# Kernel tuning notes

Measured on AMD Instinct MI355X. Metric: run time of the kernel, lower is better.

The kernel has to match this reference:

```python
import jax, jax.numpy as jnp
import numpy as np

# --- architecture constants (match init_kwargs) ---
SLEN = 104
PTILE = 8
STEP = 2
N_BANDS = 2
MAX_DET = 2
N_SRC_PARAMS = 2
ENC_C = 20
ENC_HIDDEN = 256
# dim_out_all = 0.5*D*(D+1)*(4+2*n_source_params) + 1 + D  (probs over n_sources + per-count loc/flux mean+logvar)
DIM_OUT = int(0.5 * MAX_DET * (MAX_DET + 1) * (4 + 2 * N_SRC_PARAMS)) + 1 + MAX_DET  # 27


def _p(key, shape, scale=0.02):
    return scale * jax.random.normal(key, shape, dtype=jnp.float32)


def setup_inputs() -> dict:
    key = jax.random.key(0)
    ks = jax.random.split(key, 14)
    flat_in = ENC_C * PTILE * PTILE  # 20*8*8 = 1280
    return {
        "images": jax.random.normal(ks[0], (32, N_BANDS, SLEN, SLEN), dtype=jnp.float32),
        "conv1_w": _p(ks[1], (ENC_C, N_BANDS, 3, 3)),
        "conv1_b": _p(ks[2], (ENC_C,)),
        "conv2_w": _p(ks[3], (ENC_C, ENC_C, 3, 3)),
        "conv2_b": _p(ks[4], (ENC_C,)),
        "fc1_w": _p(ks[5], (ENC_HIDDEN, flat_in)),
        "fc1_b": _p(ks[6], (ENC_HIDDEN,)),
        "fc2_w": _p(ks[7], (ENC_HIDDEN, ENC_HIDDEN)),
        "fc2_b": _p(ks[8], (ENC_HIDDEN,)),
        "fc3_w": _p(ks[9], (ENC_HIDDEN, ENC_HIDDEN)),
        "fc3_b": _p(ks[10], (ENC_HIDDEN,)),
        "fcf_w": _p(ks[11], (DIM_OUT, ENC_HIDDEN)),
        "fcf_b": _p(ks[12], (DIM_OUT,)),
    }


def _tile_images(images):
    # torch tile_images: (B, C, slen, slen) -> (B * n_ptiles, C, P, P), tiles row-major over (x, y)
    B, C = images.shape[0], images.shape[1]
    patches = jax.lax.conv_general_dilated_patches(
        images, filter_shape=(PTILE, PTILE), window_strides=(STEP, STEP), padding="VALID"
    )  # (B, C*P*P, Hn, Wn) with feature dim ordered (C, P, P)
    Hn, Wn = patches.shape[2], patches.shape[3]
    p = patches.reshape(B, C, PTILE, PTILE, Hn, Wn)
    p = p.transpose(0, 4, 5, 1, 2, 3)  # (B, Hn, Wn, C, P, P)
    return p.reshape(B * Hn * Wn, C, PTILE, PTILE)


def _conv(x, w, b):
    y = jax.lax.conv_general_dilated(
        x, w, window_strides=(1, 1), padding="SAME",
        dimension_numbers=("NCHW", "OIHW", "NCHW"),
    )
    return y + b[None, :, None, None]


def reference(images, conv1_w, conv1_b, conv2_w, conv2_b,
              fc1_w, fc1_b, fc2_w, fc2_b, fc3_w, fc3_b, fcf_w, fcf_b):
    ptiles = _tile_images(images)                       # (B*nT, C, P, P)
    h = jax.nn.relu(_conv(ptiles, conv1_w, conv1_b))    # (B*nT, 20, P, P)
    h = jax.nn.relu(_conv(h, conv2_w, conv2_b))
    h = h.reshape(h.shape[0], -1)                       # Flatten -> (B*nT, 1280)
    h = jax.nn.relu(h @ fc1_w.T + fc1_b)
    h = jax.nn.relu(h @ fc2_w.T + fc2_b)
    h = jax.nn.relu(h @ fc3_w.T + fc3_b)
    return h @ fcf_w.T + fcf_b                          # (B*nT, dim_out_all)
```

## Files before the change

kernel.cpp:

```cpp
#include <hip/hip_runtime.h>
#include <hip/hip_bf16.h>

#define NPATCH 76832
#define NBLK   601
#define K1     1280

typedef __attribute__((ext_vector_type(8))) short  short8;
typedef __attribute__((ext_vector_type(4))) float  floatx4;

__device__ __forceinline__ unsigned short f2b(float f) {
    unsigned int u = __builtin_bit_cast(unsigned int, f);
    u += 0x7FFFu + ((u >> 16) & 1u);
    return (unsigned short)(u >> 16);
}
__device__ __forceinline__ unsigned int pk2(float a, float b) {
    __hip_bfloat162 h = __float22bfloat162_rn(make_float2(a, b));
    unsigned int u;
    __builtin_memcpy(&u, &h, 4);
    return u;
}

__device__ __forceinline__ void gload_lds16(const unsigned short* g, unsigned short* l) {
    __builtin_amdgcn_global_load_lds(
        (__attribute__((address_space(1))) void*)g,
        (__attribute__((address_space(3))) void*)l,
        16, 0, 0);
}

__device__ __host__ __forceinline__ int swz8(int row, int i) {
    return (((row & 1) * 4 + i) ^ ((row >> 1) & 7));
}

__global__ void prep(const float* __restrict__ f1w, const float* __restrict__ f2w,
                     const float* __restrict__ f3w, const float* __restrict__ c1w,
                     const float* __restrict__ c2w, const float* __restrict__ ffw,
                     unsigned short* __restrict__ W1F, unsigned short* __restrict__ W2F,
                     unsigned short* __restrict__ W3F, unsigned short* __restrict__ W1T,
                     unsigned short* __restrict__ W2T, unsigned short* __restrict__ WfF) {
    int i = blockIdx.x * 256 + threadIdx.x;
    if (i < 327680) {
        int o = i / 1280, k = i - o * 1280;
        int dst = ((k >> 5) * 16 + (o >> 6) * 4 + ((o >> 4) & 3)) * 512
                + (((k >> 3) & 3) * 16 + (o & 15)) * 8 + (k & 7);
        W1F[dst] = f2b(f1w[i]);
        return;
    }
    i -= 327680;
    if (i < 65536) {
        int o = i >> 8, k = i & 255;
        int dst = ((k >> 5) * 16 + (o >> 6) * 4 + ((o >> 4) & 3)) * 512
                + (((k >> 3) & 3) * 16 + (o & 15)) * 8 + (k & 7);
        W2F[dst] = f2b(f2w[i]);
        return;
    }
    i -= 65536;
    if (i < 65536) {
        int o = i >> 8, k = i & 255;
        int dst = ((k >> 5) * 16 + (o >> 6) * 4 + ((o >> 4) & 3)) * 512
                + (((k >> 3) & 3) * 16 + (o & 15)) * 8 + (k & 7);
        W3F[dst] = f2b(f3w[i]);
        return;
    }
    i -= 65536;
    if (i < 1024) {
        int o = i >> 5, k = i & 31;
        unsigned short v = 0;
        if (o < 20 && k < 18) v = f2b(c1w[o * 18 + k]);
        W1T[(o >> 1) * 64 + swz8(o, k >> 3) * 8 + (k & 7)] = v;
        return;
    }
    i -= 1024;
    if (i < 9216) {
        int tap = i >> 10, rem = i & 1023, o = rem >> 5, c = rem & 31;
        unsigned short v = 0;
        if (o < 20 && c < 20) v = f2b(c2w[o * 180 + c * 9 + tap]);
        W2T[tap * 1024 + (o >> 1) * 64 + swz8(o, c >> 3) * 8 + (c & 7)] = v;
        return;
    }
    i -= 9216;
    if (i < 8192) {
        int o = i >> 8, k = i & 255;
        unsigned short v = (o < 27) ? f2b(ffw[o * 256 + k]) : (unsigned short)0;
        int dst = ((k >> 5) * 2 + (o >> 4)) * 512
                + (((k >> 3) & 3) * 16 + (o & 15)) * 8 + (k & 7);
        WfF[dst] = v;
    }
}

__global__ __launch_bounds__(256, 3) void conv_mfma(
    const float* __restrict__ img,
    const unsigned short* __restrict__ W1T, const float* __restrict__ b1,
    const unsigned short* __restrict__ W2T, const float* __restrict__ b2,
    unsigned short* __restrict__ X, int row0)
{
    __shared__ alignas(16) unsigned short s_buf[8 * 2048 + 64];
    __shared__ alignas(16) unsigned short s_w1t[1024];
    __shared__ alignas(16) unsigned short s_w2t[9216];
    __shared__ float s_b1[32], s_b2[32];
    constexpr int ZOFF = 8 * 2048;

    const int tid = threadIdx.x;
    for (int d = tid; d < 512; d += 256)  ((unsigned int*)s_w1t)[d] = ((const unsigned int*)W1T)[d];
    for (int d = tid; d < 4608; d += 256) ((unsigned int*)s_w2t)[d] = ((const unsigned int*)W2T)[d];
    if (tid < 32) {
        ((unsigned int*)&s_buf[ZOFF])[tid] = 0u;
        s_b1[tid] = (tid < 20) ? b1[tid] : 0.f;
        s_b2[tid] = (tid < 20) ? b2[tid] : 0.f;
    }

    const int q = tid >> 5, t = tid & 31;
    const int Pl = blockIdx.x * 8 + q;
    const int Pi = row0 + Pl;
    const bool valid = Pi < NPATCH;
    int b = 0, hi = 0, wi = 0;
    if (valid) { b = Pi / 2401; int rem = Pi - b * 2401; hi = rem / 49; wi = rem - hi * 49; }
    const int py = t >> 2, px0 = (t & 3) * 2;
    const float* ib = img + (long long)b * 21632 + (hi * 2) * 104 + (wi * 2);

    float win[2][3][4];
    #pragma unroll
    for (int c = 0; c < 2; ++c)
        #pragma unroll
        for (int dy = 0; dy < 3; ++dy) {
            int ny = py + dy - 1;
            int nyc = ny < 0 ? 0 : (ny > 7 ? 7 : ny);
            #pragma unroll
            for (int dxw = 0; dxw < 4; ++dxw) {
                int nx = px0 + dxw - 1;
                int nxc = nx < 0 ? 0 : (nx > 7 ? 7 : nx);
                win[c][dy][dxw] = ib[c * 10816 + nyc * 104 + nxc];
            }
        }

    #pragma unroll
    for (int j = 0; j < 2; ++j) {
        const int px = px0 + j, pl = py * 8 + px;
        float val[18];
        #pragma unroll
        for (int c = 0; c < 2; ++c)
            #pragma unroll
            for (int dy = 0; dy < 3; ++dy) {
                int ny = py + dy - 1;
                bool rok = valid && ((unsigned)ny < 8u);
                #pragma unroll
                for (int dx = 0; dx < 3; ++dx) {
                    int nx = px + dx - 1;
                    bool ok = rok && ((unsigned)nx < 8u);
                    val[c * 9 + dy * 3 + dx] = ok ? win[c][dy][dx + j] : 0.f;
                }
            }
        alignas(16) unsigned int au[16];
        #pragma unroll
        for (int i = 0; i < 9; ++i) au[i] = pk2(val[2 * i], val[2 * i + 1]);
        #pragma unroll
        for (int i = 9; i < 16; ++i) au[i] = 0u;
        unsigned short* base = &s_buf[q * 2048 + (pl >> 1) * 64];
        #pragma unroll
        for (int i = 0; i < 4; ++i)
            *(uint4*)&base[swz8(pl, i) * 8] = ((const uint4*)au)[i];
    }
    __syncthreads();

    const int wave = tid >> 6, lane = tid & 63;
    const int l15 = lane & 15, quad = lane >> 4;
    const int p0 = wave * 2;

    int boffB[2];
    #pragma unroll
    for (int i = 0; i < 2; ++i) {
        int oo = i * 16 + l15;
        boffB[i] = (oo >> 1) * 64 + swz8(oo, quad) * 8;
    }

    short8 a1f[2];
    #pragma unroll
    for (int mt = 0; mt < 2; ++mt) a1f[mt] = *(const short8*)&s_w1t[boffB[mt]];

    floatx4 acc1[2][2][4] = {};
    #pragma unroll
    for (int pp = 0; pp < 2; ++pp)
        #pragma unroll
        for (int nt = 0; nt < 4; ++nt) {
            int pix = nt * 16 + l15;
            short8 pf = *(const short8*)&s_buf[(p0 + pp) * 2048 + (pix >> 1) * 64 + swz8(pix, quad) * 8];
            #pragma unroll
            for (int mt = 0; mt < 2; ++mt)
                acc1[pp][mt][nt] = __builtin_amdgcn_mfma_f32_16x16x32_bf16(a1f[mt], pf, acc1[pp][mt][nt], 0, 0, 0);
        }

    float bv1[2][4];
    #pragma unroll
    for (int mt = 0; mt < 2; ++mt)
        #pragma unroll
        for (int r = 0; r < 4; ++r) bv1[mt][r] = s_b1[mt * 16 + quad * 4 + r];

    #pragma unroll
    for (int pp = 0; pp < 2; ++pp)
        #pragma unroll
        for (int mt = 0; mt < 2; ++mt)
            #pragma unroll
            for (int nt = 0; nt < 4; ++nt) {
                floatx4 v = acc1[pp][mt][nt];
                uint2 w;
                w.x = pk2(fmaxf(v[0] + bv1[mt][0], 0.f), fmaxf(v[1] + bv1[mt][1], 0.f));
                w.y = pk2(fmaxf(v[2] + bv1[mt][2], 0.f), fmaxf(v[3] + bv1[mt][3], 0.f));
                int pix = nt * 16 + l15;
                int off = (p0 + pp) * 2048 + (pix >> 1) * 64
                        + swz8(pix, mt * 2 + (quad >> 1)) * 8 + (quad & 1) * 4;
                *(uint2*)&s_buf[off] = w;
            }

    int syv[4], pxv[4];
    #pragma unroll
    for (int mt = 0; mt < 4; ++mt) { int p = mt * 16 + l15; syv[mt] = p >> 3; pxv[mt] = p & 7; }

    floatx4 acc2[2][4][2] = {};
    #pragma unroll 1
    for (int dy = 0; dy < 3; ++dy) {
        int sy[4]; bool okY[4];
        #pragma unroll
        for (int mt = 0; mt < 4; ++mt) {
            sy[mt] = syv[mt] + dy - 1;
            okY[mt] = (unsigned)sy[mt] < 8u;
        }
        #pragma unroll
        for (int dx = 0; dx < 3; ++dx) {
            const int tap = dy * 3 + dx;
            short8 bf0 = *(const short8*)&s_w2t[tap * 1024 + boffB[0]];
            short8 bf1 = *(const short8*)&s_w2t[tap * 1024 + boffB[1]];
            #pragma unroll
            for (int mt = 0; mt < 4; ++mt) {
                int sx = pxv[mt] + dx - 1;
                bool ok = okY[mt] & ((unsigned)sx < 8u);
                int ps = sy[mt] * 8 + sx;
                int offl = (ps >> 1) * 64 + swz8(ps, quad) * 8;
                #pragma unroll
                for (int pp = 0; pp < 2; ++pp) {
                    int off = ok ? ((p0 + pp) * 2048 + offl) : (ZOFF + quad * 8);
                    short8 af = *(const short8*)&s_buf[off];
                    acc2[pp][mt][0] = __builtin_amdgcn_mfma_f32_16x16x32_bf16(af, bf0, acc2[pp][mt][0], 0, 0, 0);
                    acc2[pp][mt][1] = __builtin_amdgcn_mfma_f32_16x16x32_bf16(af, bf1, acc2[pp][mt][1], 0, 0, 0);
                }
            }
        }
    }

    #pragma unroll
    for (int pp = 0; pp < 2; ++pp) {
        unsigned short* xrow = X + (long long)(blockIdx.x * 8 + p0 + pp) * K1;
        #pragma unroll
        for (int nt = 0; nt < 2; ++nt) {
            const int col = nt * 16 + l15;
            if (col < 20) {
                const float bv = s_b2[col];
                #pragma unroll
                for (int mt = 0; mt < 4; ++mt) {
                    floatx4 v = acc2[pp][mt][nt];
                    uint2 w;
                    w.x = pk2(fmaxf(v[0] + bv, 0.f), fmaxf(v[1] + bv, 0.f));
                    w.y = pk2(fmaxf(v[2] + bv, 0.f), fmaxf(v[3] + bv, 0.f));
                    *(uint2*)&xrow[col * 64 + mt * 16 + quad * 4] = w;
                }
            }
        }
    }
}

__global__ __launch_bounds__(256, 3) void fc_all(
    const unsigned short* __restrict__ X,
    const unsigned short* __restrict__ W1F, const unsigned short* __restrict__ W2F,
    const unsigned short* __restrict__ W3F, const unsigned short* __restrict__ WfF,
    const float* __restrict__ b1, const float* __restrict__ b2,
    const float* __restrict__ b3, const float* __restrict__ bf_,
    float* __restrict__ out, int row0)
{
    __shared__ alignas(16) unsigned short s_a[64 * 128];
    __shared__ alignas(16) unsigned short s_h[64 * 256];

    const int tid = threadIdx.x;
    const int m0 = blockIdx.x * 64;
    const int wave = tid >> 6, lane = tid & 63;
    const int l15 = lane & 15, quad = lane >> 4;

    floatx4 acc[4][4];
    #pragma unroll
    for (int mt = 0; mt < 4; ++mt)
        #pragma unroll
        for (int nt = 0; nt < 4; ++nt) acc[mt][nt] = floatx4{0.f, 0.f, 0.f, 0.f};

    #pragma unroll 1
    for (int kt = 0; kt < 1280; kt += 128) {
        #pragma unroll
        for (int i = 0; i < 4; ++i) {
            int g = i * 256 + tid;
            int row = g >> 4, pos = g & 15;
            int cc = (pos & 8) | ((pos & 7) ^ (row & 7));
            gload_lds16(X + (long long)(m0 + row) * 1280 + kt + cc * 8,
                        &s_a[i * 2048 + wave * 512]);
        }
        __syncthreads();
        #pragma unroll
        for (int kh = 0; kh < 4; ++kh) {
            const int khg = (kt >> 5) + kh;
            short8 af[4], bf[4];
            #pragma unroll
            for (int mt = 0; mt < 4; ++mt)
                af[mt] = *(const short8*)(W1F + (khg * 16 + wave * 4 + mt) * 512 + lane * 8);
            #pragma unroll
            for (int nt = 0; nt < 4; ++nt) {
                int row = nt * 16 + l15;
                int c = kh * 4 + quad;
                int pos = (c & 8) | ((c & 7) ^ (row & 7));
                bf[nt] = *(const short8*)&s_a[row * 128 + pos * 8];
            }
            #pragma unroll
            for (int mt = 0; mt < 4; ++mt)
                #pragma unroll
                for (int nt = 0; nt < 4; ++nt)
                    acc[mt][nt] = __builtin_amdgcn_mfma_f32_16x16x32_bf16(af[mt], bf[nt], acc[mt][nt], 0, 0, 0);
        }
        __syncthreads();
    }
    #pragma unroll
    for (int mt = 0; mt < 4; ++mt) {
        int obase = wave * 64 + mt * 16 + quad * 4;
        float v0 = b1[obase], v1 = b1[obase + 1], v2 = b1[obase + 2], v3 = b1[obase + 3];
        int clow = mt * 2 + (quad >> 1), sub = (quad & 1) * 4;
        #pragma unroll
        for (int nt = 0; nt < 4; ++nt) {
            int row = nt * 16 + l15;
            int pos = wave * 8 + (clow ^ (row & 7));
            floatx4 v = acc[mt][nt];
            uint2 w;
            w.x = pk2(fmaxf(v[0] + v0, 0.f), fmaxf(v[1] + v1, 0.f));
            w.y = pk2(fmaxf(v[2] + v2, 0.f), fmaxf(v[3] + v3, 0.f));
            *(uint2*)&s_h[row * 256 + pos * 8 + sub] = w;
        }
    }
    __syncthreads();

    #pragma unroll 1
    for (int layer = 0; layer < 2; ++layer) {
        const unsigned short* Wp = (layer == 0) ? W2F : W3F;
        const float* bp = (layer == 0) ? b2 : b3;

        #pragma unroll
        for (int mt = 0; mt < 4; ++mt)
            #pragma unroll
            for (int nt = 0; nt < 4; ++nt) acc[mt][nt] = floatx4{0.f, 0.f, 0.f, 0.f};

        #pragma unroll
        for (int it = 0; it < 8; ++it) {
            short8 af[4], bf[4];
            #pragma unroll
            for (int mt = 0; mt < 4; ++mt)
                af[mt] = *(const short8*)(Wp + (it * 16 + wave * 4 + mt) * 512 + lane * 8);
            int chi = it >> 1, clo4 = (it & 1) * 4 + quad;
            #pragma unroll
            for (int nt = 0; nt < 4; ++nt) {
                int row = nt * 16 + l15;
                bf[nt] = *(const short8*)&s_h[row * 256 + (chi * 8 + (clo4 ^ (row & 7))) * 8];
            }
            #pragma unroll
            for (int mt = 0; mt < 4; ++mt)
                #pragma unroll
                for (int nt = 0; nt < 4; ++nt)
                    acc[mt][nt] = __builtin_amdgcn_mfma_f32_16x16x32_bf16(af[mt], bf[nt], acc[mt][nt], 0, 0, 0);
        }
        __syncthreads();
        #pragma unroll
        for (int mt = 0; mt < 4; ++mt) {
            int obase = wave * 64 + mt * 16 + quad * 4;
            float v0 = bp[obase], v1 = bp[obase + 1], v2 = bp[obase + 2], v3 = bp[obase + 3];
            int clow = mt * 2 + (quad >> 1), sub = (quad & 1) * 4;
            #pragma unroll
            for (int nt = 0; nt < 4; ++nt) {
                int row = nt * 16 + l15;
                int pos = wave * 8 + (clow ^ (row & 7));
                floatx4 v = acc[mt][nt];
                uint2 w;
                w.x = pk2(fmaxf(v[0] + v0, 0.f), fmaxf(v[1] + v1, 0.f));
                w.y = pk2(fmaxf(v[2] + v2, 0.f), fmaxf(v[3] + v3, 0.f));
                *(uint2*)&s_h[row * 256 + pos * 8 + sub] = w;
            }
        }
        __syncthreads();
    }

    floatx4 accf[2] = {};
    const int myrow = wave * 16 + l15;
    #pragma unroll
    for (int w8 = 0; w8 < 8; ++w8) {
        int chi = w8 >> 1, clo = (w8 & 1) * 4 + quad;
        short8 bfr = *(const short8*)&s_h[myrow * 256 + (chi * 8 + (clo ^ (myrow & 7))) * 8];
        #pragma unroll
        for (int mt = 0; mt < 2; ++mt) {
            short8 afr = *(const short8*)(WfF + (w8 * 2 + mt) * 512 + lane * 8);
            accf[mt] = __builtin_amdgcn_mfma_f32_16x16x32_bf16(afr, bfr, accf[mt], 0, 0, 0);
        }
    }
    const int grow = row0 + m0 + myrow;
    if (grow < NPATCH) {
        #pragma unroll
        for (int mt = 0; mt < 2; ++mt) {
            #pragma unroll
            for (int r = 0; r < 4; ++r) {
                int o = mt * 16 + quad * 4 + r;
                if (o < 27)
                    out[(long long)grow * 27 + o] = accf[mt][r] + bf_[o];
            }
        }
    }
}

extern "C" void kernel_launch(void* const* d_in, const int* in_sizes, int n_in,
                              void* d_out, int out_size, void* d_ws, size_t ws_size,
                              hipStream_t stream) {
    const float* images = (const float*)d_in[0];
    const float* c1w = (const float*)d_in[1];
    const float* c1b = (const float*)d_in[2];
    const float* c2w = (const float*)d_in[3];
    const float* c2b = (const float*)d_in[4];
    const float* f1w = (const float*)d_in[5];
    const float* f1b = (const float*)d_in[6];
    const float* f2w = (const float*)d_in[7];
    const float* f2b_ = (const float*)d_in[8];
    const float* f3w = (const float*)d_in[9];
    const float* f3b = (const float*)d_in[10];
    const float* ffw = (const float*)d_in[11];
    const float* ffb = (const float*)d_in[12];

    const long long W1_E = 327680, W2_E = 65536, W3_E = 65536;
    const long long W1T_E = 1024, W2T_E = 9216, WF_E = 8192;
    const long long WB = (W1_E + W2_E + W3_E + W1T_E + W2T_E + WF_E) * 2;
    char* ws = (char*)d_ws;
    unsigned short* W1F = (unsigned short*)ws;
    unsigned short* W2F = W1F + W1_E;
    unsigned short* W3F = W2F + W2_E;
    unsigned short* W1T = W3F + W3_E;
    unsigned short* W2T = W1T + W1T_E;
    unsigned short* WfF = W2T + W2T_E;
    unsigned short* X   = (unsigned short*)(ws + WB);

    long long avail = (long long)ws_size - WB - 256;
    int nb_max = (int)(avail / 327680LL);
    if (nb_max < 1) nb_max = 1;
    if (nb_max > NBLK) nb_max = NBLK;
    int nchunks = (NBLK + nb_max - 1) / nb_max;
    int nb_even = (NBLK + nchunks - 1) / nchunks;

    prep<<<1864, 256, 0, stream>>>(f1w, f2w, f3w, c1w, c2w, ffw, W1F, W2F, W3F, W1T, W2T, WfF);

    for (int b0 = 0; b0 < NBLK; b0 += nb_even) {
        int nb = NBLK - b0; if (nb > nb_even) nb = nb_even;
        int row0 = b0 * 128;
        int rows = nb * 128;

        conv_mfma<<<rows / 8, 256, 0, stream>>>(images, W1T, c1b, W2T, c2b, X, row0);
        fc_all<<<rows / 64, 256, 0, stream>>>(X, W1F, W2F, W3F, WfF,
                                              f1b, f2b_, f3b, ffb, (float*)d_out, row0);
    }
}
```

Measured before the change: 323.5 us.

## Load conv weights from global in fragment order; double-buffer fc1 LDS tiles

Conv weights are now pre-packed in per-lane MFMA fragment order and read straight from global memory (cache), which removes the per-block LDS staging of about 20KB. That frees LDS so launch bounds can rise to 4 blocks per SM. The fc1 K-loop now double-buffers 64-wide K tiles in LDS, prefetching the next tile with global_load_lds while computing the current one, and uses one barrier per iteration instead of two. The trade-offs are global or L1 latency on each weight fragment read in the conv kernel and more loop iterations in fc1.

```diff
diff --git a/kernel.cpp b/kernel.cpp
--- a/kernel.cpp
+++ b/kernel.cpp
@@ -35,8 +35,8 @@
                      const float* __restrict__ f3w, const float* __restrict__ c1w,
                      const float* __restrict__ c2w, const float* __restrict__ ffw,
                      unsigned short* __restrict__ W1F, unsigned short* __restrict__ W2F,
-                     unsigned short* __restrict__ W3F, unsigned short* __restrict__ W1T,
-                     unsigned short* __restrict__ W2T, unsigned short* __restrict__ WfF) {
+                     unsigned short* __restrict__ W3F, unsigned short* __restrict__ W1c,
+                     unsigned short* __restrict__ W2c, unsigned short* __restrict__ WfF) {
     int i = blockIdx.x * 256 + threadIdx.x;
     if (i < 327680) {
         int o = i / 1280, k = i - o * 1280;
@@ -63,18 +63,17 @@
     }
     i -= 65536;
     if (i < 1024) {
-        int o = i >> 5, k = i & 31;
-        unsigned short v = 0;
-        if (o < 20 && k < 18) v = f2b(c1w[o * 18 + k]);
-        W1T[(o >> 1) * 64 + swz8(o, k >> 3) * 8 + (k & 7)] = v;
+        int mt = i >> 9, rem = i & 511, lane = rem >> 3, j = rem & 7;
+        int o = mt * 16 + (lane & 15), k = (lane >> 4) * 8 + j;
+        W1c[i] = (o < 20 && k < 18) ? f2b(c1w[o * 18 + k]) : (unsigned short)0;
         return;
     }
     i -= 1024;
     if (i < 9216) {
-        int tap = i >> 10, rem = i & 1023, o = rem >> 5, c = rem & 31;
-        unsigned short v = 0;
-        if (o < 20 && c < 20) v = f2b(c2w[o * 180 + c * 9 + tap]);
-        W2T[tap * 1024 + (o >> 1) * 64 + swz8(o, c >> 3) * 8 + (c & 7)] = v;
+        int tap = i >> 10, rem = i & 1023, nt = rem >> 9;
+        int rem2 = rem & 511, lane = rem2 >> 3, j = rem2 & 7;
+        int o = nt * 16 + (lane & 15), c = (lane >> 4) * 8 + j;
+        W2c[i] = (o < 20 && c < 20) ? f2b(c2w[o * 180 + c * 9 + tap]) : (unsigned short)0;
         return;
     }
     i -= 9216;
@@ -87,21 +86,17 @@
     }
 }
 
-__global__ __launch_bounds__(256, 3) void conv_mfma(
+__global__ __launch_bounds__(256, 4) void conv_mfma(
     const float* __restrict__ img,
-    const unsigned short* __restrict__ W1T, const float* __restrict__ b1,
-    const unsigned short* __restrict__ W2T, const float* __restrict__ b2,
+    const unsigned short* __restrict__ W1c, const float* __restrict__ b1,
+    const unsigned short* __restrict__ W2c, const float* __restrict__ b2,
     unsigned short* __restrict__ X, int row0)
 {
     __shared__ alignas(16) unsigned short s_buf[8 * 2048 + 64];
-    __shared__ alignas(16) unsigned short s_w1t[1024];
-    __shared__ alignas(16) unsigned short s_w2t[9216];
     __shared__ float s_b1[32], s_b2[32];
     constexpr int ZOFF = 8 * 2048;
 
     const int tid = threadIdx.x;
-    for (int d = tid; d < 512; d += 256)  ((unsigned int*)s_w1t)[d] = ((const unsigned int*)W1T)[d];
-    for (int d = tid; d < 4608; d += 256) ((unsigned int*)s_w2t)[d] = ((const unsigned int*)W2T)[d];
     if (tid < 32) {
         ((unsigned int*)&s_buf[ZOFF])[tid] = 0u;
         s_b1[tid] = (tid < 20) ? b1[tid] : 0.f;
@@ -165,16 +160,10 @@
     const int l15 = lane & 15, quad = lane >> 4;
     const int p0 = wave * 2;
 
-    int boffB[2];
-    #pragma unroll
-    for (int i = 0; i < 2; ++i) {
-        int oo = i * 16 + l15;
-        boffB[i] = (oo >> 1) * 64 + swz8(oo, quad) * 8;
-    }
-
     short8 a1f[2];
     #pragma unroll
-    for (int mt = 0; mt < 2; ++mt) a1f[mt] = *(const short8*)&s_w1t[boffB[mt]];
+    for (int mt = 0; mt < 2; ++mt)
+        a1f[mt] = *(const short8*)(W1c + mt * 512 + lane * 8);
 
     floatx4 acc1[2][2][4] = {};
     #pragma unroll
@@ -226,8 +215,9 @@
         #pragma unroll
         for (int dx = 0; dx < 3; ++dx) {
             const int tap = dy * 3 + dx;
-            short8 bf0 = *(const short8*)&s_w2t[tap * 1024 + boffB[0]];
-            short8 bf1 = *(const short8*)&s_w2t[tap * 1024 + boffB[1]];
+            const unsigned short* wt = W2c + tap * 1024 + lane * 8;
+            short8 bf0 = *(const short8*)(wt);
+            short8 bf1 = *(const short8*)(wt + 512);
             #pragma unroll
             for (int mt = 0; mt < 4; ++mt) {
                 int sx = pxv[mt] + dx - 1;
@@ -274,7 +264,7 @@
     const float* __restrict__ b3, const float* __restrict__ bf_,
     float* __restrict__ out, int row0)
 {
-    __shared__ alignas(16) unsigned short s_a[64 * 128];
+    __shared__ alignas(16) unsigned short s_a[2][64 * 64];
     __shared__ alignas(16) unsigned short s_h[64 * 256];
 
     const int tid = threadIdx.x;
@@ -288,20 +278,32 @@
         #pragma unroll
         for (int nt = 0; nt < 4; ++nt) acc[mt][nt] = floatx4{0.f, 0.f, 0.f, 0.f};
 
+    #pragma unroll
+    for (int i = 0; i < 2; ++i) {
+        int cb = i * 256 + wave * 64;
+        int ci = cb + lane;
+        int row = ci >> 3, c = ci & 7;
+        gload_lds16(X + (long long)(m0 + row) * 1280 + (c ^ (row & 7)) * 8, &s_a[0][cb * 8]);
+    }
+
     #pragma unroll 1
-    for (int kt = 0; kt < 1280; kt += 128) {
-        #pragma unroll
-        for (int i = 0; i < 4; ++i) {
-            int g = i * 256 + tid;
-            int row = g >> 4, pos = g & 15;
-            int cc = (pos & 8) | ((pos & 7) ^ (row & 7));
-            gload_lds16(X + (long long)(m0 + row) * 1280 + kt + cc * 8,
-                        &s_a[i * 2048 + wave * 512]);
-        }
+    for (int it = 0; it < 20; ++it) {
         __syncthreads();
-        #pragma unroll
-        for (int kh = 0; kh < 4; ++kh) {
-            const int khg = (kt >> 5) + kh;
+        const int cur = it & 1;
+        if (it + 1 < 20) {
+            const int nxt = (it + 1) & 1;
+            #pragma unroll
+            for (int i = 0; i < 2; ++i) {
+                int cb = i * 256 + wave * 64;
+                int ci = cb + lane;
+                int row = ci >> 3, c = ci & 7;
+                gload_lds16(X + (long long)(m0 + row) * 1280 + (it + 1) * 64 + (c ^ (row & 7)) * 8,
+                            &s_a[nxt][cb * 8]);
+            }
+        }
+        #pragma unroll
+        for (int kh = 0; kh < 2; ++kh) {
+            const int khg = it * 2 + kh;
             short8 af[4], bf[4];
             #pragma unroll
             for (int mt = 0; mt < 4; ++mt)
@@ -310,8 +312,7 @@
             for (int nt = 0; nt < 4; ++nt) {
                 int row = nt * 16 + l15;
                 int c = kh * 4 + quad;
-                int pos = (c & 8) | ((c & 7) ^ (row & 7));
-                bf[nt] = *(const short8*)&s_a[row * 128 + pos * 8];
+                bf[nt] = *(const short8*)&s_a[cur][row * 64 + (c ^ (row & 7)) * 8];
             }
             #pragma unroll
             for (int mt = 0; mt < 4; ++mt)
@@ -319,7 +320,6 @@
                 for (int nt = 0; nt < 4; ++nt)
                     acc[mt][nt] = __builtin_amdgcn_mfma_f32_16x16x32_bf16(af[mt], bf[nt], acc[mt][nt], 0, 0, 0);
         }
-        __syncthreads();
     }
     #pragma unroll
     for (int mt = 0; mt < 4; ++mt) {
@@ -431,15 +431,15 @@
     const float* ffb = (const float*)d_in[12];
 
     const long long W1_E = 327680, W2_E = 65536, W3_E = 65536;
-    const long long W1T_E = 1024, W2T_E = 9216, WF_E = 8192;
-    const long long WB = (W1_E + W2_E + W3_E + W1T_E + W2T_E + WF_E) * 2;
+    const long long W1c_E = 1024, W2c_E = 9216, WF_E = 8192;
+    const long long WB = (W1_E + W2_E + W3_E + W1c_E + W2c_E + WF_E) * 2;
     char* ws = (char*)d_ws;
     unsigned short* W1F = (unsigned short*)ws;
     unsigned short* W2F = W1F + W1_E;
     unsigned short* W3F = W2F + W2_E;
-    unsigned short* W1T = W3F + W3_E;
-    unsigned short* W2T = W1T + W1T_E;
-    unsigned short* WfF = W2T + W2T_E;
+    unsigned short* W1c = W3F + W3_E;
+    unsigned short* W2c = W1c + W1c_E;
+    unsigned short* WfF = W2c + W2c_E;
     unsigned short* X   = (unsigned short*)(ws + WB);
 
     long long avail = (long long)ws_size - WB - 256;
@@ -449,14 +449,14 @@
     int nchunks = (NBLK + nb_max - 1) / nb_max;
     int nb_even = (NBLK + nchunks - 1) / nchunks;
 
-    prep<<<1864, 256, 0, stream>>>(f1w, f2w, f3w, c1w, c2w, ffw, W1F, W2F, W3F, W1T, W2T, WfF);
+    prep<<<1864, 256, 0, stream>>>(f1w, f2w, f3w, c1w, c2w, ffw, W1F, W2F, W3F, W1c, W2c, WfF);
 
     for (int b0 = 0; b0 < NBLK; b0 += nb_even) {
         int nb = NBLK - b0; if (nb > nb_even) nb = nb_even;
         int row0 = b0 * 128;
         int rows = nb * 128;
 
-        conv_mfma<<<rows / 8, 256, 0, stream>>>(images, W1T, c1b, W2T, c2b, X, row0);
+        conv_mfma<<<rows / 8, 256, 0, stream>>>(images, W1c, c1b, W2c, c2b, X, row0);
         fc_all<<<rows / 64, 256, 0, stream>>>(X, W1F, W2F, W3F, WfF,
                                               f1b, f2b_, f3b, ffb, (float*)d_out, row0);
     }
```

New measurement: 356.5 us. 10.2% more time.
